# Kernel optimization log

Hardware: AMD Instinct MI355X
Metric: run time of the kernel (lower is better)

The kernel has to match this reference:

```python
import jax, jax.numpy as jnp
import numpy as np

N = 100000
E = 1600000
IN, HID, OUT = 128, 256, 47


def _glorot(key, shape):
    fan_in, fan_out = shape
    lim = np.sqrt(6.0 / (fan_in + fan_out))
    return jax.random.uniform(key, shape, jnp.float32, -lim, lim)


def setup_inputs() -> dict:
    key = jax.random.key(0)
    ks = jax.random.split(key, 12)
    x = jax.random.normal(ks[0], (N, IN), jnp.float32)
    src = jax.random.randint(ks[1], (E,), 0, N, jnp.int32)
    dst = jax.random.randint(ks[2], (E,), 0, N, jnp.int32)
    dims = [(IN, HID), (HID, HID), (HID, OUT)]
    inp = {"x": x, "src": src, "dst": dst}
    for i, (di, do) in enumerate(dims, 1):
        inp[f"w_self{i}"] = _glorot(ks[2 + 3 * i - 2], (di, do))
        inp[f"w_neigh{i}"] = _glorot(ks[2 + 3 * i - 1], (di, do))
        inp[f"b{i}"] = jnp.zeros((do,), jnp.float32)
    return inp


def sage_conv(x, src, dst, w_self, w_neigh, b):
    n = x.shape[0]
    msg = x[src]                                              # [E, d] gather
    summed = jax.ops.segment_sum(msg, dst, num_segments=n)    # [N, d]
    deg = jax.ops.segment_sum(jnp.ones((src.shape[0],), x.dtype), dst, num_segments=n)
    h_neigh = summed / jnp.maximum(deg, 1.0)[:, None]         # mean aggregate
    return x @ w_self + h_neigh @ w_neigh + b


def reference(x, src, dst, w_self1, w_neigh1, b1, w_self2, w_neigh2, b2, w_self3, w_neigh3, b3):
    h = sage_conv(x, src, dst, w_self1, w_neigh1, b1)
    h = jax.nn.relu(h)  # dropout = identity in eval mode
    h = sage_conv(h, src, dst, w_self2, w_neigh2, b2)
    h = jax.nn.relu(h)
    h = sage_conv(h, src, dst, w_self3, w_neigh3, b3)
    return h
```

## Files before the change

### kernel.cpp

```cpp
#include <hip/hip_runtime.h>

#define N_NODES 100000
#define N_EDGES 1600000

typedef __attribute__((ext_vector_type(8))) _Float16 half8;
typedef __attribute__((ext_vector_type(4))) _Float16 half4v;
typedef __attribute__((ext_vector_type(4))) float floatx4;


__global__ void deg_rank(const int* __restrict__ dst, int* __restrict__ deg,
                         int* __restrict__ rank, int e) {
    int i = blockIdx.x * blockDim.x + threadIdx.x;
    if (i < e) rank[i] = atomicAdd(&deg[dst[i]], 1);
}


__global__ __launch_bounds__(256) void scan_partial(const int* __restrict__ deg,
                                                    int* __restrict__ bsum, int n) {
    __shared__ int wsum[4];
    int t = threadIdx.x;
    int base = blockIdx.x * 2048 + t * 8;
    int tsum = 0;
    #pragma unroll
    for (int k = 0; k < 8; ++k) {
        int idx = base + k;
        tsum += (idx < n) ? deg[idx] : 0;
    }
    #pragma unroll
    for (int d = 1; d < 64; d <<= 1) tsum += __shfl_xor(tsum, d, 64);
    if ((t & 63) == 0) wsum[t >> 6] = tsum;
    __syncthreads();
    if (t == 0) bsum[blockIdx.x] = wsum[0] + wsum[1] + wsum[2] + wsum[3];
}

__global__ void scan_blocksums(const int* __restrict__ bsum, int* __restrict__ bbase, int nb) {
    int t = threadIdx.x;
    int v = (t < nb) ? bsum[t] : 0;
    int s = v;
    #pragma unroll
    for (int d = 1; d < 64; d <<= 1) {
        int u = __shfl_up(s, d, 64);
        if (t >= d) s += u;
    }
    if (t < nb) bbase[t] = s - v;
    if (t == 63) bbase[nb] = s;
}

__global__ __launch_bounds__(256) void scan_write(const int* __restrict__ deg,
                                                  const int* __restrict__ bbase,
                                                  int* __restrict__ offs, int n, int nb) {
    __shared__ int wsum[4];
    int t = threadIdx.x;
    int lane = t & 63, w = t >> 6;
    int base = blockIdx.x * 2048 + t * 8;
    int v[8];
    #pragma unroll
    for (int k = 0; k < 8; ++k) {
        int idx = base + k;
        v[k] = (idx < n) ? deg[idx] : 0;
    }
    int tsum = 0;
    #pragma unroll
    for (int k = 0; k < 8; ++k) { int x = v[k]; v[k] = tsum; tsum += x; }
    int s = tsum;
    #pragma unroll
    for (int d = 1; d < 64; d <<= 1) {
        int u = __shfl_up(s, d, 64);
        if (lane >= d) s += u;
    }
    if (lane == 63) wsum[w] = s;
    __syncthreads();
    int wb = 0;
    for (int j = 0; j < w; ++j) wb += wsum[j];
    int texcl = bbase[blockIdx.x] + wb + (s - tsum);
    #pragma unroll
    for (int k = 0; k < 8; ++k) {
        int idx = base + k;
        if (idx < n) offs[idx] = texcl + v[k];
    }
    if (blockIdx.x == 0 && t == 0) offs[n] = bbase[nb];
}

__global__ void fill_csr2(const int* __restrict__ src, const int* __restrict__ dst,
                          const int* __restrict__ offs, const int* __restrict__ rank,
                          int* __restrict__ csr, int e) {
    int i = blockIdx.x * blockDim.x + threadIdx.x;
    if (i < e) csr[offs[dst[i]] + rank[i]] = src[i];
}


__global__ void cvt_f16(const float4* __restrict__ in, half4v* __restrict__ oh, int n4) {
    int i = blockIdx.x * blockDim.x + threadIdx.x;
    if (i >= n4) return;
    float4 v = in[i];
    half4v h;
    h[0] = (_Float16)v.x; h[1] = (_Float16)v.y;
    h[2] = (_Float16)v.z; h[3] = (_Float16)v.w;
    oh[i] = h;
}


__global__ void prep_all(const float* __restrict__ ws1, const float* __restrict__ wn1,
                         const float* __restrict__ ws2, const float* __restrict__ wn2,
                         const float* __restrict__ ws3, const float* __restrict__ wn3,
                         _Float16* __restrict__ o1s, _Float16* __restrict__ o1n,
                         _Float16* __restrict__ o2s, _Float16* __restrict__ o2n,
                         _Float16* __restrict__ o3c) {
    int i = blockIdx.x * blockDim.x + threadIdx.x;
    if (i < 65536) {
        const float* W = (i < 32768) ? ws1 : wn1;
        _Float16* O = (i < 32768) ? o1s : o1n;
        int j = i & 32767;
        int nn = j >> 7, k = j & 127;
        O[j] = (_Float16)W[k * 256 + nn];
    } else if (i < 196608) {
        int j = i - 65536;
        const float* W = (j < 65536) ? ws2 : wn2;
        _Float16* O = (j < 65536) ? o2s : o2n;
        j &= 65535;
        int nn = j >> 8, k = j & 255;
        O[j] = (_Float16)W[k * 256 + nn];
    } else if (i < 221184) {
        int j = i - 196608;
        const float* W = (j < 12288) ? ws3 : wn3;
        _Float16* O = o3c + ((j < 12288) ? 0 : 12288);
        j = (j < 12288) ? j : j - 12288;
        int nn = j >> 8, k = j & 255;
        O[j] = (nn < 47) ? (_Float16)W[k * 47 + nn] : (_Float16)0.f;
    }
}


__global__ __launch_bounds__(256) void agg256h(const _Float16* __restrict__ Hh,
                                               const int* __restrict__ csr,
                                               const int* __restrict__ offs,
                                               _Float16* __restrict__ Ph, int n) {
    int node = blockIdx.x * 4 + (threadIdx.x >> 6);
    int lane = threadIdx.x & 63;
    int hf = lane >> 5;
    int sl = lane & 31;
    if (node >= n) return;
    int e0 = offs[node], e1 = offs[node + 1];
    float a[8] = {0.f, 0.f, 0.f, 0.f, 0.f, 0.f, 0.f, 0.f};
    int e = e0;
    for (; e + 8 <= e1; e += 8) {
        int s0 = csr[e + hf];
        int s1 = csr[e + 2 + hf];
        int s2 = csr[e + 4 + hf];
        int s3 = csr[e + 6 + hf];
        half8 u0 = ((const half8*)(Hh + (size_t)s0 * 256))[sl];
        half8 u1 = ((const half8*)(Hh + (size_t)s1 * 256))[sl];
        half8 u2 = ((const half8*)(Hh + (size_t)s2 * 256))[sl];
        half8 u3 = ((const half8*)(Hh + (size_t)s3 * 256))[sl];
        #pragma unroll
        for (int j = 0; j < 8; ++j) a[j] += (float)u0[j];
        #pragma unroll
        for (int j = 0; j < 8; ++j) a[j] += (float)u1[j];
        #pragma unroll
        for (int j = 0; j < 8; ++j) a[j] += (float)u2[j];
        #pragma unroll
        for (int j = 0; j < 8; ++j) a[j] += (float)u3[j];
    }
    for (; e + 2 <= e1; e += 2) {
        int s = csr[e + hf];
        half8 u = ((const half8*)(Hh + (size_t)s * 256))[sl];
        #pragma unroll
        for (int j = 0; j < 8; ++j) a[j] += (float)u[j];
    }
    if (e < e1 && hf == 0) {
        int s = csr[e];
        half8 u = ((const half8*)(Hh + (size_t)s * 256))[sl];
        #pragma unroll
        for (int j = 0; j < 8; ++j) a[j] += (float)u[j];
    }
    #pragma unroll
    for (int j = 0; j < 8; ++j) a[j] += __shfl_xor(a[j], 32);
    if (hf == 0) {
        float inv = 1.0f / fmaxf((float)(e1 - e0), 1.0f);
        half8 rh;
        #pragma unroll
        for (int j = 0; j < 8; ++j) rh[j] = (_Float16)(a[j] * inv);
        ((half8*)(Ph + (size_t)node * 256))[sl] = rh;
    }
}

__global__ __launch_bounds__(256) void agg128h(const _Float16* __restrict__ xh,
                                               const int* __restrict__ csr,
                                               const int* __restrict__ offs,
                                               _Float16* __restrict__ Ph, int n) {
    int node = blockIdx.x * 4 + (threadIdx.x >> 6);
    int lane = threadIdx.x & 63;
    int qtr = lane >> 4;
    int sl = lane & 15;
    if (node >= n) return;
    int e0 = offs[node], e1 = offs[node + 1];
    float a[8] = {0.f, 0.f, 0.f, 0.f, 0.f, 0.f, 0.f, 0.f};
    int e = e0;
    for (; e + 8 <= e1; e += 8) {
        int s0 = csr[e + qtr];
        int s1 = csr[e + 4 + qtr];
        half8 u0 = ((const half8*)(xh + (size_t)s0 * 128))[sl];
        half8 u1 = ((const half8*)(xh + (size_t)s1 * 128))[sl];
        #pragma unroll
        for (int j = 0; j < 8; ++j) a[j] += (float)u0[j];
        #pragma unroll
        for (int j = 0; j < 8; ++j) a[j] += (float)u1[j];
    }
    for (; e + 4 <= e1; e += 4) {
        int s = csr[e + qtr];
        half8 u = ((const half8*)(xh + (size_t)s * 128))[sl];
        #pragma unroll
        for (int j = 0; j < 8; ++j) a[j] += (float)u[j];
    }
    int rem = e1 - e;
    if (qtr < rem) {
        int s = csr[e + qtr];
        half8 u = ((const half8*)(xh + (size_t)s * 128))[sl];
        #pragma unroll
        for (int j = 0; j < 8; ++j) a[j] += (float)u[j];
    }
    #pragma unroll
    for (int j = 0; j < 8; ++j) {
        a[j] += __shfl_xor(a[j], 16);
        a[j] += __shfl_xor(a[j], 32);
    }
    if (lane < 16) {
        float inv = 1.0f / fmaxf((float)(e1 - e0), 1.0f);
        half8 rh;
        #pragma unroll
        for (int j = 0; j < 8; ++j) rh[j] = (_Float16)(a[j] * inv);
        ((half8*)(Ph + (size_t)node * 128))[sl] = rh;
    }
}

__global__ __launch_bounds__(256) void agg_l3(const _Float16* __restrict__ Y,
                                              const float* __restrict__ S,
                                              const int* __restrict__ csr,
                                              const int* __restrict__ offs,
                                              float* __restrict__ out, int n) {
    int node = blockIdx.x * 4 + (threadIdx.x >> 6);
    int lane = threadIdx.x & 63;
    int qtr = lane >> 4;
    int sl = lane & 15;
    int c = sl < 12 ? sl : 11;
    if (node >= n) return;
    int e0 = offs[node], e1 = offs[node + 1];
    float a0 = 0.f, a1 = 0.f, a2 = 0.f, a3 = 0.f;
    int e = e0;
    for (; e + 8 <= e1; e += 8) {
        int s0 = csr[e + qtr];
        int s1 = csr[e + 4 + qtr];
        half4v f0 = ((const half4v*)(Y + (size_t)s0 * 48))[c];
        half4v f1 = ((const half4v*)(Y + (size_t)s1 * 48))[c];
        a0 += (float)f0[0] + (float)f1[0];
        a1 += (float)f0[1] + (float)f1[1];
        a2 += (float)f0[2] + (float)f1[2];
        a3 += (float)f0[3] + (float)f1[3];
    }
    for (; e + 4 <= e1; e += 4) {
        int s = csr[e + qtr];
        half4v f = ((const half4v*)(Y + (size_t)s * 48))[c];
        a0 += (float)f[0]; a1 += (float)f[1]; a2 += (float)f[2]; a3 += (float)f[3];
    }
    int rem = e1 - e;
    if (qtr < rem) {
        int s = csr[e + qtr];
        half4v f = ((const half4v*)(Y + (size_t)s * 48))[c];
        a0 += (float)f[0]; a1 += (float)f[1]; a2 += (float)f[2]; a3 += (float)f[3];
    }
    a0 += __shfl_xor(a0, 16); a0 += __shfl_xor(a0, 32);
    a1 += __shfl_xor(a1, 16); a1 += __shfl_xor(a1, 32);
    a2 += __shfl_xor(a2, 16); a2 += __shfl_xor(a2, 32);
    a3 += __shfl_xor(a3, 16); a3 += __shfl_xor(a3, 32);
    if (lane < 12) {
        float inv = 1.0f / fmaxf((float)(e1 - e0), 1.0f);
        float4 sv = ((const float4*)(S + (size_t)node * 48))[c];
        float r[4] = {sv.x + a0 * inv, sv.y + a1 * inv, sv.z + a2 * inv, sv.w + a3 * inv};
        #pragma unroll
        for (int k = 0; k < 4; ++k) {
            int col = c * 4 + k;
            if (col < 47) out[(size_t)node * 47 + col] = r[k];
        }
    }
}


template <int NTILES, int OUTFMT>
__global__ __launch_bounds__(256, 2) void gemm_mfma(
    const _Float16* __restrict__ A1h, const _Float16* __restrict__ A2h,
    const _Float16* __restrict__ W1, const _Float16* __restrict__ W2,
    const float* __restrict__ bias, float* __restrict__ outS, _Float16* __restrict__ outY,
    _Float16* __restrict__ outh, int n, int K, int dout, int relu, int phases) {
    constexpr int NPAD = NTILES * 16;
    constexpr int LDT = 36;
    __shared__ _Float16 Bs[NPAD * LDT];

    const int t = threadIdx.x;
    const int bm = blockIdx.x * 128;
    const int lane = t & 63;
    const int w = t >> 6;
    const int quad = lane >> 4;
    const int tl = lane & 15;
    const int r0 = bm + w * 32 + tl;
    const int r1 = r0 + 16;

    floatx4 acc[2][NTILES];
    #pragma unroll
    for (int i = 0; i < 2; ++i)
        #pragma unroll
        for (int j = 0; j < NTILES; ++j) acc[i][j] = (floatx4){0.f, 0.f, 0.f, 0.f};

    const int spp = K >> 5;
    const int nsteps = phases * spp;

    half8 pb0, pb1, pb2, pb3;
    half8 pah0 = {0}, pah1 = {0};

    if (t < NPAD) {
        const half8* p = (const half8*)(W1 + (size_t)t * K);
        pb0 = p[0]; pb1 = p[1]; pb2 = p[2]; pb3 = p[3];
    }
    {
        int kq = quad * 8;
        if (r0 < n) pah0 = *(const half8*)(A1h + (size_t)r0 * K + kq);
        if (r1 < n) pah1 = *(const half8*)(A1h + (size_t)r1 * K + kq);
    }

    for (int s = 0; s < nsteps; ++s) {
        __syncthreads();
        if (t < NPAD) {
            *(half8*)&Bs[t * LDT + 0]  = pb0;
            *(half8*)&Bs[t * LDT + 8]  = pb1;
            *(half8*)&Bs[t * LDT + 16] = pb2;
            *(half8*)&Bs[t * LDT + 24] = pb3;
        }
        __syncthreads();
        half8 ah0 = pah0, ah1 = pah1;
        if (s + 1 < nsteps) {
            int s2 = s + 1;
            int ph2 = (s2 >= spp) ? 1 : 0;
            int k02 = (ph2 ? s2 - spp : s2) << 5;
            if (t < NPAD) {
                const _Float16* W = ph2 ? W2 : W1;
                const half8* p = (const half8*)(W + (size_t)t * K + k02);
                pb0 = p[0]; pb1 = p[1]; pb2 = p[2]; pb3 = p[3];
            }
            const _Float16* Ah = ph2 ? A2h : A1h;
            int kq = k02 + quad * 8;
            pah0 = (half8){0}; pah1 = (half8){0};
            if (r0 < n) pah0 = *(const half8*)(Ah + (size_t)r0 * K + kq);
            if (r1 < n) pah1 = *(const half8*)(Ah + (size_t)r1 * K + kq);
        }
        #pragma unroll
        for (int nt = 0; nt < NTILES; ++nt) {
            half8 bh = *(const half8*)&Bs[(nt * 16 + tl) * LDT + quad * 8];
            acc[0][nt] = __builtin_amdgcn_mfma_f32_16x16x32_f16(ah0, bh, acc[0][nt], 0, 0, 0);
            acc[1][nt] = __builtin_amdgcn_mfma_f32_16x16x32_f16(ah1, bh, acc[1][nt], 0, 0, 0);
        }
    }

    #pragma unroll
    for (int mt = 0; mt < 2; ++mt) {
        #pragma unroll
        for (int nt = 0; nt < NTILES; ++nt) {
            int gc = nt * 16 + tl;
            if (OUTFMT == 1 && gc >= dout) continue;
            #pragma unroll
            for (int r = 0; r < 4; ++r) {
                int gr = bm + w * 32 + mt * 16 + quad * 4 + r;
                if (gr >= n) continue;
                float v = acc[mt][nt][r];
                if (OUTFMT == 1) {
                    v += bias[gc];
                    if (relu) v = fmaxf(v, 0.f);
                    outh[(size_t)gr * 256 + gc] = (_Float16)v;
                } else {
                    if (gc < 48) {
                        v += (gc < 47) ? bias[gc] : 0.f;
                        outS[(size_t)gr * 48 + gc] = v;
                    } else {
                        outY[(size_t)gr * 48 + (gc - 48)] = (_Float16)v;
                    }
                }
            }
        }
    }
}

extern "C" void kernel_launch(void* const* d_in, const int* in_sizes, int n_in,
                              void* d_out, int out_size, void* d_ws, size_t ws_size,
                              hipStream_t stream) {
    (void)in_sizes; (void)n_in; (void)out_size; (void)ws_size;
    const int N = N_NODES, E = N_EDGES;
    const float* x = (const float*)d_in[0];
    const int* src = (const int*)d_in[1];
    const int* dst = (const int*)d_in[2];
    const float* w_self1 = (const float*)d_in[3];
    const float* w_neigh1 = (const float*)d_in[4];
    const float* b1 = (const float*)d_in[5];
    const float* w_self2 = (const float*)d_in[6];
    const float* w_neigh2 = (const float*)d_in[7];
    const float* b2 = (const float*)d_in[8];
    const float* w_self3 = (const float*)d_in[9];
    const float* w_neigh3 = (const float*)d_in[10];
    const float* b3 = (const float*)d_in[11];
    float* out = (float*)d_out;

    _Float16* Ph = (_Float16*)d_ws;
    _Float16* Hh = Ph + (size_t)N * 256;
    int* deg = (int*)(Hh + (size_t)N * 256);
    int* offs = deg + N;
    int* csr = offs + N + 4;
    _Float16* wbuf = (_Float16*)(csr + E);
    _Float16* w1s = wbuf;
    _Float16* w1n = w1s + 32768;
    _Float16* w2s = w1n + 32768;
    _Float16* w2n = w2s + 65536;
    _Float16* w3c = w2n + 65536;
    int* bsum = (int*)(w3c + 24576);
    int* bbase = bsum + 64;
    int* rank = (int*)Ph;
    _Float16* xh = Ph + (size_t)N * 128;
    float* S = (float*)Ph;
    _Float16* Y = (_Float16*)(S + (size_t)N * 48);

    const int NB = (N + 2047) / 2048;

    hipMemsetAsync(deg, 0, N * sizeof(int), stream);
    deg_rank<<<(E + 255) / 256, 256, 0, stream>>>(dst, deg, rank, E);
    scan_partial<<<NB, 256, 0, stream>>>(deg, bsum, N);
    scan_blocksums<<<1, 64, 0, stream>>>(bsum, bbase, NB);
    scan_write<<<NB, 256, 0, stream>>>(deg, bbase, offs, N, NB);
    fill_csr2<<<(E + 255) / 256, 256, 0, stream>>>(src, dst, offs, rank, csr, E);

    cvt_f16<<<(N * 128 / 4 + 255) / 256, 256, 0, stream>>>((const float4*)x, (half4v*)xh,
                                                           N * 128 / 4);
    prep_all<<<(221184 + 255) / 256, 256, 0, stream>>>(w_self1, w_neigh1, w_self2, w_neigh2,
                                                       w_self3, w_neigh3, w1s, w1n, w2s, w2n,
                                                       w3c);

    int gemmGrid = (N + 127) / 128;
    int aggGrid = (N + 3) / 4;

    agg128h<<<aggGrid, 256, 0, stream>>>(xh, csr, offs, Ph, N);
    gemm_mfma<16, 1><<<gemmGrid, 256, 0, stream>>>(xh, Ph, w1s, w1n, b1, nullptr, nullptr,
                                                   Hh, N, 128, 256, 1, 2);
    agg256h<<<aggGrid, 256, 0, stream>>>(Hh, csr, offs, Ph, N);
    gemm_mfma<16, 1><<<gemmGrid, 256, 0, stream>>>(Hh, Ph, w2s, w2n, b2, nullptr, nullptr,
                                                   Hh, N, 256, 256, 1, 2);
    gemm_mfma<6, 2><<<gemmGrid, 256, 0, stream>>>(Hh, nullptr, w3c, nullptr, b3, S, Y,
                                                  nullptr, N, 256, 96, 0, 1);
    agg_l3<<<aggGrid, 256, 0, stream>>>(Y, S, csr, offs, out, N);
}
```

Before: 647.0 us.

## Split 256-wide hidden features into two 128-column planes for aggregation

Hidden activations are now stored as two planar [N,128] halves instead of row-major [N,256]. The layer-2 aggregation runs as two passes of a single 128-wide gather kernel, so each pass gathers from a smaller working set that fits cache better. The GEMM load and store indexing is rewritten for the planar layout, and the 128-wide aggregator gains a 16-edge unrolled loop for more loads in flight. The cost is reading CSR indices and offsets twice and one extra kernel launch.

New measurement: 641.5 us. No clear change (-0.9%).

```diff
diff --git a/kernel.cpp b/kernel.cpp
--- a/kernel.cpp
+++ b/kernel.cpp
@@ -131,63 +131,10 @@
 }
 
 
-__global__ __launch_bounds__(256) void agg256h(const _Float16* __restrict__ Hh,
-                                               const int* __restrict__ csr,
-                                               const int* __restrict__ offs,
-                                               _Float16* __restrict__ Ph, int n) {
-    int node = blockIdx.x * 4 + (threadIdx.x >> 6);
-    int lane = threadIdx.x & 63;
-    int hf = lane >> 5;
-    int sl = lane & 31;
-    if (node >= n) return;
-    int e0 = offs[node], e1 = offs[node + 1];
-    float a[8] = {0.f, 0.f, 0.f, 0.f, 0.f, 0.f, 0.f, 0.f};
-    int e = e0;
-    for (; e + 8 <= e1; e += 8) {
-        int s0 = csr[e + hf];
-        int s1 = csr[e + 2 + hf];
-        int s2 = csr[e + 4 + hf];
-        int s3 = csr[e + 6 + hf];
-        half8 u0 = ((const half8*)(Hh + (size_t)s0 * 256))[sl];
-        half8 u1 = ((const half8*)(Hh + (size_t)s1 * 256))[sl];
-        half8 u2 = ((const half8*)(Hh + (size_t)s2 * 256))[sl];
-        half8 u3 = ((const half8*)(Hh + (size_t)s3 * 256))[sl];
-        #pragma unroll
-        for (int j = 0; j < 8; ++j) a[j] += (float)u0[j];
-        #pragma unroll
-        for (int j = 0; j < 8; ++j) a[j] += (float)u1[j];
-        #pragma unroll
-        for (int j = 0; j < 8; ++j) a[j] += (float)u2[j];
-        #pragma unroll
-        for (int j = 0; j < 8; ++j) a[j] += (float)u3[j];
-    }
-    for (; e + 2 <= e1; e += 2) {
-        int s = csr[e + hf];
-        half8 u = ((const half8*)(Hh + (size_t)s * 256))[sl];
-        #pragma unroll
-        for (int j = 0; j < 8; ++j) a[j] += (float)u[j];
-    }
-    if (e < e1 && hf == 0) {
-        int s = csr[e];
-        half8 u = ((const half8*)(Hh + (size_t)s * 256))[sl];
-        #pragma unroll
-        for (int j = 0; j < 8; ++j) a[j] += (float)u[j];
-    }
-    #pragma unroll
-    for (int j = 0; j < 8; ++j) a[j] += __shfl_xor(a[j], 32);
-    if (hf == 0) {
-        float inv = 1.0f / fmaxf((float)(e1 - e0), 1.0f);
-        half8 rh;
-        #pragma unroll
-        for (int j = 0; j < 8; ++j) rh[j] = (_Float16)(a[j] * inv);
-        ((half8*)(Ph + (size_t)node * 256))[sl] = rh;
-    }
-}
-
-__global__ __launch_bounds__(256) void agg128h(const _Float16* __restrict__ xh,
-                                               const int* __restrict__ csr,
-                                               const int* __restrict__ offs,
-                                               _Float16* __restrict__ Ph, int n) {
+__global__ __launch_bounds__(256) void aggP(const _Float16* __restrict__ Xp,
+                                            const int* __restrict__ csr,
+                                            const int* __restrict__ offs,
+                                            _Float16* __restrict__ Pp, int n) {
     int node = blockIdx.x * 4 + (threadIdx.x >> 6);
     int lane = threadIdx.x & 63;
     int qtr = lane >> 4;
@@ -196,11 +143,29 @@
     int e0 = offs[node], e1 = offs[node + 1];
     float a[8] = {0.f, 0.f, 0.f, 0.f, 0.f, 0.f, 0.f, 0.f};
     int e = e0;
+    for (; e + 16 <= e1; e += 16) {
+        int s0 = csr[e + qtr];
+        int s1 = csr[e + 4 + qtr];
+        int s2 = csr[e + 8 + qtr];
+        int s3 = csr[e + 12 + qtr];
+        half8 u0 = ((const half8*)(Xp + (size_t)s0 * 128))[sl];
+        half8 u1 = ((const half8*)(Xp + (size_t)s1 * 128))[sl];
+        half8 u2 = ((const half8*)(Xp + (size_t)s2 * 128))[sl];
+        half8 u3 = ((const half8*)(Xp + (size_t)s3 * 128))[sl];
+        #pragma unroll
+        for (int j = 0; j < 8; ++j) a[j] += (float)u0[j];
+        #pragma unroll
+        for (int j = 0; j < 8; ++j) a[j] += (float)u1[j];
+        #pragma unroll
+        for (int j = 0; j < 8; ++j) a[j] += (float)u2[j];
+        #pragma unroll
+        for (int j = 0; j < 8; ++j) a[j] += (float)u3[j];
+    }
     for (; e + 8 <= e1; e += 8) {
         int s0 = csr[e + qtr];
         int s1 = csr[e + 4 + qtr];
-        half8 u0 = ((const half8*)(xh + (size_t)s0 * 128))[sl];
-        half8 u1 = ((const half8*)(xh + (size_t)s1 * 128))[sl];
+        half8 u0 = ((const half8*)(Xp + (size_t)s0 * 128))[sl];
+        half8 u1 = ((const half8*)(Xp + (size_t)s1 * 128))[sl];
         #pragma unroll
         for (int j = 0; j < 8; ++j) a[j] += (float)u0[j];
         #pragma unroll
@@ -208,14 +173,14 @@
     }
     for (; e + 4 <= e1; e += 4) {
         int s = csr[e + qtr];
-        half8 u = ((const half8*)(xh + (size_t)s * 128))[sl];
+        half8 u = ((const half8*)(Xp + (size_t)s * 128))[sl];
         #pragma unroll
         for (int j = 0; j < 8; ++j) a[j] += (float)u[j];
     }
     int rem = e1 - e;
     if (qtr < rem) {
         int s = csr[e + qtr];
-        half8 u = ((const half8*)(xh + (size_t)s * 128))[sl];
+        half8 u = ((const half8*)(Xp + (size_t)s * 128))[sl];
         #pragma unroll
         for (int j = 0; j < 8; ++j) a[j] += (float)u[j];
     }
@@ -229,7 +194,7 @@
         half8 rh;
         #pragma unroll
         for (int j = 0; j < 8; ++j) rh[j] = (_Float16)(a[j] * inv);
-        ((half8*)(Ph + (size_t)node * 128))[sl] = rh;
+        ((half8*)(Pp + (size_t)node * 128))[sl] = rh;
     }
 }
 
@@ -303,6 +268,7 @@
     const int tl = lane & 15;
     const int r0 = bm + w * 32 + tl;
     const int r1 = r0 + 16;
+    const size_t PS = (size_t)n * 128;
 
     floatx4 acc[2][NTILES];
     #pragma unroll
@@ -322,8 +288,8 @@
     }
     {
         int kq = quad * 8;
-        if (r0 < n) pah0 = *(const half8*)(A1h + (size_t)r0 * K + kq);
-        if (r1 < n) pah1 = *(const half8*)(A1h + (size_t)r1 * K + kq);
+        if (r0 < n) pah0 = *(const half8*)(A1h + (size_t)r0 * 128 + kq);
+        if (r1 < n) pah1 = *(const half8*)(A1h + (size_t)r1 * 128 + kq);
     }
 
     for (int s = 0; s < nsteps; ++s) {
@@ -347,9 +313,10 @@
             }
             const _Float16* Ah = ph2 ? A2h : A1h;
             int kq = k02 + quad * 8;
+            const _Float16* Ab = Ah + ((kq >> 7) ? PS : (size_t)0) + (kq & 127);
             pah0 = (half8){0}; pah1 = (half8){0};
-            if (r0 < n) pah0 = *(const half8*)(Ah + (size_t)r0 * K + kq);
-            if (r1 < n) pah1 = *(const half8*)(Ah + (size_t)r1 * K + kq);
+            if (r0 < n) pah0 = *(const half8*)(Ab + (size_t)r0 * 128);
+            if (r1 < n) pah1 = *(const half8*)(Ab + (size_t)r1 * 128);
         }
         #pragma unroll
         for (int nt = 0; nt < NTILES; ++nt) {
@@ -373,7 +340,7 @@
                 if (OUTFMT == 1) {
                     v += bias[gc];
                     if (relu) v = fmaxf(v, 0.f);
-                    outh[(size_t)gr * 256 + gc] = (_Float16)v;
+                    outh[(size_t)(gc >> 7) * PS + (size_t)gr * 128 + (gc & 127)] = (_Float16)v;
                 } else {
                     if (gc < 48) {
                         v += (gc < 47) ? bias[gc] : 0.f;
@@ -442,10 +409,11 @@
     int gemmGrid = (N + 127) / 128;
     int aggGrid = (N + 3) / 4;
 
-    agg128h<<<aggGrid, 256, 0, stream>>>(xh, csr, offs, Ph, N);
+    aggP<<<aggGrid, 256, 0, stream>>>(xh, csr, offs, Ph, N);
     gemm_mfma<16, 1><<<gemmGrid, 256, 0, stream>>>(xh, Ph, w1s, w1n, b1, nullptr, nullptr,
                                                    Hh, N, 128, 256, 1, 2);
-    agg256h<<<aggGrid, 256, 0, stream>>>(Hh, csr, offs, Ph, N);
+    aggP<<<aggGrid, 256, 0, stream>>>(Hh, csr, offs, Ph, N);
+    aggP<<<aggGrid, 256, 0, stream>>>(Hh + (size_t)N * 128, csr, offs, Ph + (size_t)N * 128, N);
     gemm_mfma<16, 1><<<gemmGrid, 256, 0, stream>>>(Hh, Ph, w2s, w2n, b2, nullptr, nullptr,
                                                    Hh, N, 256, 256, 1, 2);
     gemm_mfma<6, 2><<<gemmGrid, 256, 0, stream>>>(Hh, nullptr, w3c, nullptr, b3, S, Y,
```
